# Optimization experiments

Hardware: AMD Instinct MI355X
Metric: run time of the kernel (lower is better)

## Reference

```python
import jax, jax.numpy as jnp
import numpy as np

N_NODES = 50000
N_EDGES = 800000
HID = 256
ATOM_F = 256
BOND_F = 128
BN_EPS = 1e-5


def setup_inputs() -> dict:
    key = jax.random.key(0)
    ks = jax.random.split(key, 8)
    x = jax.random.normal(ks[0], (N_NODES, ATOM_F), dtype=jnp.float32)
    w = jax.random.normal(ks[1], (N_EDGES, BOND_F), dtype=jnp.float32)
    dst = jax.random.randint(ks[2], (N_EDGES,), 0, N_NODES, dtype=jnp.int32)
    # Linear weights (PyTorch layout: [out, in]) scaled like kaiming-uniform-ish
    W_atom = jax.random.normal(ks[3], (HID, ATOM_F), dtype=jnp.float32) / np.sqrt(ATOM_F)
    b_atom = jax.random.normal(ks[4], (HID,), dtype=jnp.float32) * 0.01
    W_bond = jax.random.normal(ks[5], (HID, BOND_F), dtype=jnp.float32) / np.sqrt(BOND_F)
    b_bond = jax.random.normal(ks[6], (HID,), dtype=jnp.float32) * 0.01
    gamma = jnp.ones((HID,), dtype=jnp.float32)
    beta = jnp.zeros((HID,), dtype=jnp.float32)
    return {"x": x, "w": w, "dst": dst, "W_atom": W_atom, "b_atom": b_atom,
            "W_bond": W_bond, "b_bond": b_bond, "gamma": gamma, "beta": beta}


def reference(x, w, dst, W_atom, b_atom, W_bond, b_bond, gamma, beta):
    # Per-edge linear projection of bond features: [E, HID]
    h_edge = jnp.einsum('ef,hf->eh', w, W_bond) + b_bond
    # Scatter-sum messages into destination nodes: [N, HID]
    agg = jax.ops.segment_sum(h_edge, dst, num_segments=x.shape[0])
    # Node linear + add aggregated messages
    h = agg + jnp.einsum('nf,hf->nh', x, W_atom) + b_atom
    # ReLU then BatchNorm1d (training mode: biased batch stats, affine)
    h = jax.nn.relu(h)
    mean = jnp.mean(h, axis=0)
    var = jnp.mean(jnp.square(h - mean), axis=0)
    out = (h - mean) * jax.lax.rsqrt(var + BN_EPS) * gamma + beta
    return out
```

## Files before the change

### kernel.cpp

```cpp
#include <hip/hip_runtime.h>

#define NN 50000
#define NE 800000
#define HIDN 256
#define AF 256
#define BF 128
#define KT 384
#define NCHUNK 1563
#define GG 256
#define MAXDEG 128

typedef __attribute__((ext_vector_type(8))) short short8;
typedef __attribute__((ext_vector_type(4))) float f32x4;
typedef __attribute__((ext_vector_type(2))) float f32x2;

__device__ __forceinline__ unsigned short f2bf(float f) {
    union { float f; unsigned int u; } c; c.f = f;
    unsigned int u = c.u;
    return (unsigned short)((u + 0x7FFFu + ((u >> 16) & 1u)) >> 16);
}
__device__ __forceinline__ float bf2f(unsigned short u) {
    union { unsigned int u; float f; } c; c.u = (unsigned int)u << 16;
    return c.f;
}

__global__ __launch_bounds__(256) void k_sortW(const int4* __restrict__ dst4,
        int* __restrict__ cursor, int* __restrict__ sortedEdge,
        const float* __restrict__ Wa, const float* __restrict__ Wb,
        unsigned short* __restrict__ Wc) {
    const int i = blockIdx.x * 256 + threadIdx.x;
    if (i < NE / 4) {
        const int4 d = dst4[i];
        const int e = i * 4;
        int p;
        p = atomicAdd(cursor + d.x, 1); if (p < MAXDEG) sortedEdge[d.x * MAXDEG + p] = e;
        p = atomicAdd(cursor + d.y, 1); if (p < MAXDEG) sortedEdge[d.y * MAXDEG + p] = e + 1;
        p = atomicAdd(cursor + d.z, 1); if (p < MAXDEG) sortedEdge[d.z * MAXDEG + p] = e + 2;
        p = atomicAdd(cursor + d.w, 1); if (p < MAXDEG) sortedEdge[d.w * MAXDEG + p] = e + 3;
    }
    if (blockIdx.x < 48) {
        const int gid = blockIdx.x * 256 + threadIdx.x;
        const int j = gid / 48, cb = gid % 48;
        const float* src = (cb < 32) ? (Wa + j * AF + cb * 8) : (Wb + j * BF + (cb - 32) * 8);
        f32x4 a = reinterpret_cast<const f32x4*>(src)[0];
        f32x4 b = reinterpret_cast<const f32x4*>(src)[1];
        short8 s;
        s[0] = f2bf(a[0]); s[1] = f2bf(a[1]); s[2] = f2bf(a[2]); s[3] = f2bf(a[3]);
        s[4] = f2bf(b[0]); s[5] = f2bf(b[1]); s[6] = f2bf(b[2]); s[7] = f2bf(b[3]);
        *reinterpret_cast<short8*>(Wc + j * KT + cb * 8) = s;
    }
}

__global__ __launch_bounds__(256) void k_gather(const float* __restrict__ w,
        const int* __restrict__ sortedEdge, const int* __restrict__ cursor,
        unsigned short* __restrict__ agg) {
    const int node = blockIdx.x * 4 + (threadIdx.x >> 6);
    const int lane = threadIdx.x & 63;
    if (node >= NN) return;
    const int start = node * MAXDEG;
    const int degn = min(cursor[node], MAXDEG);
    const f32x2* __restrict__ w2 = reinterpret_cast<const f32x2*>(w);
    float ax = 0.f, ay = 0.f;
    for (int base = 0; base < degn; base += 64) {
        const int m = min(64, degn - base);
        int eid = 0;
        if (lane < m) eid = sortedEdge[start + base + lane];
        int i = 0;
        for (; i + 8 <= m; i += 8) {
            int e0 = __shfl(eid, i + 0), e1 = __shfl(eid, i + 1);
            int e2 = __shfl(eid, i + 2), e3 = __shfl(eid, i + 3);
            int e4 = __shfl(eid, i + 4), e5 = __shfl(eid, i + 5);
            int e6 = __shfl(eid, i + 6), e7 = __shfl(eid, i + 7);
            f32x2 v0 = __builtin_nontemporal_load(&w2[(size_t)e0 * 64 + lane]);
            f32x2 v1 = __builtin_nontemporal_load(&w2[(size_t)e1 * 64 + lane]);
            f32x2 v2 = __builtin_nontemporal_load(&w2[(size_t)e2 * 64 + lane]);
            f32x2 v3 = __builtin_nontemporal_load(&w2[(size_t)e3 * 64 + lane]);
            f32x2 v4 = __builtin_nontemporal_load(&w2[(size_t)e4 * 64 + lane]);
            f32x2 v5 = __builtin_nontemporal_load(&w2[(size_t)e5 * 64 + lane]);
            f32x2 v6 = __builtin_nontemporal_load(&w2[(size_t)e6 * 64 + lane]);
            f32x2 v7 = __builtin_nontemporal_load(&w2[(size_t)e7 * 64 + lane]);
            ax += ((v0.x + v1.x) + (v2.x + v3.x)) + ((v4.x + v5.x) + (v6.x + v7.x));
            ay += ((v0.y + v1.y) + (v2.y + v3.y)) + ((v4.y + v5.y) + (v6.y + v7.y));
        }
        for (; i < m; ++i) {
            int e = __shfl(eid, i);
            f32x2 v = __builtin_nontemporal_load(&w2[(size_t)e * 64 + lane]);
            ax += v.x;
            ay += v.y;
        }
    }
    unsigned int pack = (unsigned int)f2bf(ax) | ((unsigned int)f2bf(ay) << 16);
    *reinterpret_cast<unsigned int*>(agg + (size_t)node * BF + lane * 2) = pack;
}

#define LOADCHUNK(P, ch) do { \
    const int base_ = (ch) * 32; \
    const int g0_ = base_ + xr0, g1_ = g0_ + 16, g2_ = base_ + gr_; \
    if (g0_ < NN) { const f32x4* s_ = reinterpret_cast<const f32x4*>(x + (size_t)g0_ * AF + xkb * 8); \
        P##xa0 = __builtin_nontemporal_load(s_); P##xb0 = __builtin_nontemporal_load(s_ + 1); } \
    else { P##xa0 = f32x4{0.f,0.f,0.f,0.f}; P##xb0 = f32x4{0.f,0.f,0.f,0.f}; } \
    if (g1_ < NN) { const f32x4* s_ = reinterpret_cast<const f32x4*>(x + (size_t)g1_ * AF + xkb * 8); \
        P##xa1 = __builtin_nontemporal_load(s_); P##xb1 = __builtin_nontemporal_load(s_ + 1); } \
    else { P##xa1 = f32x4{0.f,0.f,0.f,0.f}; P##xb1 = f32x4{0.f,0.f,0.f,0.f}; } \
    if (g2_ < NN) { P##ga = *reinterpret_cast<const short8*>(agg + (size_t)g2_ * BF + gkb * 8); } \
    else { P##ga = short8{0,0,0,0,0,0,0,0}; } \
} while (0)

#define WRITECHUNK(P, BUF) do { \
    short8 s_; \
    s_[0]=f2bf(P##xa0[0]); s_[1]=f2bf(P##xa0[1]); s_[2]=f2bf(P##xa0[2]); s_[3]=f2bf(P##xa0[3]); \
    s_[4]=f2bf(P##xb0[0]); s_[5]=f2bf(P##xb0[1]); s_[6]=f2bf(P##xb0[2]); s_[7]=f2bf(P##xb0[3]); \
    *reinterpret_cast<short8*>((BUF) + xr0 * KT + ((xkb ^ (xr0 & 7)) << 3)) = s_; \
    s_[0]=f2bf(P##xa1[0]); s_[1]=f2bf(P##xa1[1]); s_[2]=f2bf(P##xa1[2]); s_[3]=f2bf(P##xa1[3]); \
    s_[4]=f2bf(P##xb1[0]); s_[5]=f2bf(P##xb1[1]); s_[6]=f2bf(P##xb1[2]); s_[7]=f2bf(P##xb1[3]); \
    *reinterpret_cast<short8*>((BUF) + (xr0 + 16) * KT + ((xkb ^ (xr0 & 7)) << 3)) = s_; \
    *reinterpret_cast<short8*>((BUF) + gr_ * KT + (((32 + gkb) ^ (gr_ & 7)) << 3)) = P##ga; \
} while (0)

__global__ __launch_bounds__(512, 1) void k_gemm(const float* __restrict__ x,
        const unsigned short* __restrict__ agg, const int* __restrict__ cnt,
        const unsigned short* __restrict__ Wc, const float* __restrict__ b_atom,
        const float* __restrict__ b_bond, unsigned short* __restrict__ hbf,
        float* __restrict__ colsum, float* __restrict__ colsumsq) {
    __shared__ unsigned short As0[32 * KT];
    __shared__ unsigned short As1[32 * KT];

    const int tid = threadIdx.x;
    const int wid = tid >> 6, lane = tid & 63;
    const int lrow = lane & 15, lk = lane >> 4;
    const int colb = wid * 32;

    short8 breg[2][12];
    #pragma unroll
    for (int t = 0; t < 2; ++t)
        #pragma unroll
        for (int kt = 0; kt < 12; ++kt)
            breg[t][kt] = *reinterpret_cast<const short8*>(
                Wc + (size_t)(colb + t * 16 + lrow) * KT + kt * 32 + lk * 8);

    const float ba0 = b_atom[colb + lrow],      bb0 = b_bond[colb + lrow];
    const float ba1 = b_atom[colb + 16 + lrow], bb1 = b_bond[colb + 16 + lrow];

    f32x4 Axa0, Axb0, Axa1, Axb1; short8 Aga;
    f32x4 Bxa0, Bxb0, Bxa1, Bxb1; short8 Bga;
    const int xr0 = tid >> 5, xkb = tid & 31;
    const int gr_ = tid >> 4, gkb = tid & 15;

    float st0 = 0.f, st20 = 0.f, st1 = 0.f, st21 = 0.f;

    auto compute = [&](int chunk, const unsigned short* A) {
        f32x4 a00{0.f,0.f,0.f,0.f}, a01{0.f,0.f,0.f,0.f};
        f32x4 a10{0.f,0.f,0.f,0.f}, a11{0.f,0.f,0.f,0.f};
        #pragma unroll
        for (int kt = 0; kt < 12; ++kt) {
            const int kb = kt * 4 + lk;
            short8 f0 = *reinterpret_cast<const short8*>(
                A + lrow * KT + ((kb ^ (lrow & 7)) << 3));
            short8 f1 = *reinterpret_cast<const short8*>(
                A + (16 + lrow) * KT + ((kb ^ (lrow & 7)) << 3));
            a00 = __builtin_amdgcn_mfma_f32_16x16x32_bf16(f0, breg[0][kt], a00, 0, 0, 0);
            a01 = __builtin_amdgcn_mfma_f32_16x16x32_bf16(f1, breg[0][kt], a01, 0, 0, 0);
            a10 = __builtin_amdgcn_mfma_f32_16x16x32_bf16(f0, breg[1][kt], a10, 0, 0, 0);
            a11 = __builtin_amdgcn_mfma_f32_16x16x32_bf16(f1, breg[1][kt], a11, 0, 0, 0);
        }
        #pragma unroll
        for (int rb = 0; rb < 2; ++rb) {
            const int row0 = chunk * 32 + rb * 16 + lk * 4;
            const f32x4 accA = rb ? a01 : a00;
            const f32x4 accB = rb ? a11 : a10;
            #pragma unroll
            for (int r2 = 0; r2 < 4; ++r2) {
                const int gr = row0 + r2;
                if (gr < NN) {
                    const float dg = (float)cnt[gr];
                    const float v0 = fmaxf(accA[r2] + ba0 + dg * bb0, 0.f);
                    const float v1 = fmaxf(accB[r2] + ba1 + dg * bb1, 0.f);
                    hbf[(size_t)gr * HIDN + colb + lrow]      = f2bf(v0);
                    hbf[(size_t)gr * HIDN + colb + 16 + lrow] = f2bf(v1);
                    st0 += v0; st20 += v0 * v0;
                    st1 += v1; st21 += v1 * v1;
                }
            }
        }
    };

    LOADCHUNK(A, blockIdx.x);
    WRITECHUNK(A, As0);
    LOADCHUNK(B, blockIdx.x + GG);
    asm volatile("s_waitcnt lgkmcnt(0)" ::: "memory");
    __builtin_amdgcn_s_barrier();

    int chunk = blockIdx.x;
    while (true) {
        WRITECHUNK(B, As1);
        LOADCHUNK(A, chunk + 2 * GG);
        compute(chunk, As0);
        asm volatile("s_waitcnt lgkmcnt(0)" ::: "memory");
        __builtin_amdgcn_s_barrier();
        chunk += GG;
        if (chunk >= NCHUNK) break;

        WRITECHUNK(A, As0);
        LOADCHUNK(B, chunk + 2 * GG);
        compute(chunk, As1);
        asm volatile("s_waitcnt lgkmcnt(0)" ::: "memory");
        __builtin_amdgcn_s_barrier();
        chunk += GG;
        if (chunk >= NCHUNK) break;
    }

    st0 += __shfl_xor(st0, 16); st0 += __shfl_xor(st0, 32);
    st20 += __shfl_xor(st20, 16); st20 += __shfl_xor(st20, 32);
    st1 += __shfl_xor(st1, 16); st1 += __shfl_xor(st1, 32);
    st21 += __shfl_xor(st21, 16); st21 += __shfl_xor(st21, 32);
    if (lane < 16) {
        atomicAdd(colsum + colb + lane, st0);
        atomicAdd(colsumsq + colb + lane, st20);
        atomicAdd(colsum + colb + 16 + lane, st1);
        atomicAdd(colsumsq + colb + 16 + lane, st21);
    }
}

__global__ __launch_bounds__(256) void k_bn(const unsigned short* __restrict__ hbf,
        const float* __restrict__ colsum, const float* __restrict__ colsumsq,
        const float* __restrict__ gamma, const float* __restrict__ beta,
        float* __restrict__ out) {
    __shared__ float scs[HIDN], shs[HIDN];
    const int t = threadIdx.x;
    {
        const float mean = colsum[t] * (1.f / NN);
        const float var = colsumsq[t] * (1.f / NN) - mean * mean;
        const float sc = gamma[t] * rsqrtf(var + 1e-5f);
        scs[t] = sc;
        shs[t] = beta[t] - mean * sc;
    }
    __syncthreads();
    const int total = NN * HIDN / 8;
    const short8* __restrict__ h8 = reinterpret_cast<const short8*>(hbf);
    f32x4* __restrict__ out4 = reinterpret_cast<f32x4*>(out);
    for (int gid = blockIdx.x * 256 + t; gid < total; gid += gridDim.x * 256) {
        const short8 v = __builtin_nontemporal_load(&h8[gid]);
        const int c = (gid & 31) * 8;
        f32x4 r0, r1;
        #pragma unroll
        for (int k = 0; k < 4; ++k)
            r0[k] = fmaf(bf2f((unsigned short)v[k]), scs[c + k], shs[c + k]);
        #pragma unroll
        for (int k = 0; k < 4; ++k)
            r1[k] = fmaf(bf2f((unsigned short)v[4 + k]), scs[c + 4 + k], shs[c + 4 + k]);
        __builtin_nontemporal_store(r0, &out4[gid * 2]);
        __builtin_nontemporal_store(r1, &out4[gid * 2 + 1]);
    }
}

extern "C" void kernel_launch(void* const* d_in, const int* in_sizes, int n_in,
                              void* d_out, int out_size, void* d_ws, size_t ws_size,
                              hipStream_t stream) {
    const float* x      = (const float*)d_in[0];
    const float* w      = (const float*)d_in[1];
    const int*   dst    = (const int*)d_in[2];
    const float* W_atom = (const float*)d_in[3];
    const float* b_atom = (const float*)d_in[4];
    const float* W_bond = (const float*)d_in[5];
    const float* b_bond = (const float*)d_in[6];
    const float* gamma  = (const float*)d_in[7];
    const float* beta   = (const float*)d_in[8];
    float* out = (float*)d_out;

    int*   cursor     = (int*)d_ws;
    float* colsum     = (float*)(cursor + NN);
    float* colsumsq   = colsum + HIDN;
    int*   sortedEdge = (int*)(colsumsq + HIDN);
    unsigned short* Wc  = (unsigned short*)(sortedEdge + (size_t)NN * MAXDEG);
    unsigned short* agg = Wc + (size_t)HIDN * KT;
    unsigned short* hbf = agg + (size_t)NN * BF;

    hipMemsetAsync(d_ws, 0, (size_t)(NN + 2 * HIDN) * 4, stream);

    k_sortW<<<(NE / 4 + 255) / 256, 256, 0, stream>>>((const int4*)dst, cursor,
                                                      sortedEdge, W_atom, W_bond, Wc);
    k_gather<<<(NN + 3) / 4, 256, 0, stream>>>(w, sortedEdge, cursor, agg);
    k_gemm<<<GG, 512, 0, stream>>>(x, agg, cursor, Wc, b_atom, b_bond,
                                   hbf, colsum, colsumsq);
    k_bn<<<2048, 256, 0, stream>>>(hbf, colsum, colsumsq, gamma, beta, out);
}
```

Baseline: 196.5 us.

## Fuse gather, GEMM and batchnorm into one persistent kernel with grid barriers

Replaces the separate gather, GEMM and BN kernels with a single persistent kernel of 256 blocks. Phases are separated by software grid barriers built on atomic counters. The aim is to remove two kernel launches and their tail idle gaps. In exchange, the gather phase runs with only 256 blocks of 8 waves at one block per CU, which may expose less memory-level parallelism than the original 12500-block launch. It also relies on every block being co-resident for the spin barrier.

```diff
diff --git a/kernel.cpp b/kernel.cpp
--- a/kernel.cpp
+++ b/kernel.cpp
@@ -7,7 +7,7 @@
 #define BF 128
 #define KT 384
 #define NCHUNK 1563
-#define GG 256
+#define NBLK 256
 #define MAXDEG 128
 
 typedef __attribute__((ext_vector_type(8))) short short8;
@@ -22,6 +22,18 @@
 __device__ __forceinline__ float bf2f(unsigned short u) {
     union { unsigned int u; float f; } c; c.u = (unsigned int)u << 16;
     return c.f;
+}
+
+__device__ __forceinline__ void grid_barrier(int* ctr) {
+    __syncthreads();
+    __threadfence();
+    if (threadIdx.x == 0) {
+        __hip_atomic_fetch_add(ctr, 1, __ATOMIC_ACQ_REL, __HIP_MEMORY_SCOPE_AGENT);
+        while (__hip_atomic_load(ctr, __ATOMIC_ACQUIRE, __HIP_MEMORY_SCOPE_AGENT) < NBLK) {
+            __builtin_amdgcn_s_sleep(2);
+        }
+    }
+    __syncthreads();
 }
 
 __global__ __launch_bounds__(256) void k_sortW(const int4* __restrict__ dst4,
@@ -51,48 +63,6 @@
     }
 }
 
-__global__ __launch_bounds__(256) void k_gather(const float* __restrict__ w,
-        const int* __restrict__ sortedEdge, const int* __restrict__ cursor,
-        unsigned short* __restrict__ agg) {
-    const int node = blockIdx.x * 4 + (threadIdx.x >> 6);
-    const int lane = threadIdx.x & 63;
-    if (node >= NN) return;
-    const int start = node * MAXDEG;
-    const int degn = min(cursor[node], MAXDEG);
-    const f32x2* __restrict__ w2 = reinterpret_cast<const f32x2*>(w);
-    float ax = 0.f, ay = 0.f;
-    for (int base = 0; base < degn; base += 64) {
-        const int m = min(64, degn - base);
-        int eid = 0;
-        if (lane < m) eid = sortedEdge[start + base + lane];
-        int i = 0;
-        for (; i + 8 <= m; i += 8) {
-            int e0 = __shfl(eid, i + 0), e1 = __shfl(eid, i + 1);
-            int e2 = __shfl(eid, i + 2), e3 = __shfl(eid, i + 3);
-            int e4 = __shfl(eid, i + 4), e5 = __shfl(eid, i + 5);
-            int e6 = __shfl(eid, i + 6), e7 = __shfl(eid, i + 7);
-            f32x2 v0 = __builtin_nontemporal_load(&w2[(size_t)e0 * 64 + lane]);
-            f32x2 v1 = __builtin_nontemporal_load(&w2[(size_t)e1 * 64 + lane]);
-            f32x2 v2 = __builtin_nontemporal_load(&w2[(size_t)e2 * 64 + lane]);
-            f32x2 v3 = __builtin_nontemporal_load(&w2[(size_t)e3 * 64 + lane]);
-            f32x2 v4 = __builtin_nontemporal_load(&w2[(size_t)e4 * 64 + lane]);
-            f32x2 v5 = __builtin_nontemporal_load(&w2[(size_t)e5 * 64 + lane]);
-            f32x2 v6 = __builtin_nontemporal_load(&w2[(size_t)e6 * 64 + lane]);
-            f32x2 v7 = __builtin_nontemporal_load(&w2[(size_t)e7 * 64 + lane]);
-            ax += ((v0.x + v1.x) + (v2.x + v3.x)) + ((v4.x + v5.x) + (v6.x + v7.x));
-            ay += ((v0.y + v1.y) + (v2.y + v3.y)) + ((v4.y + v5.y) + (v6.y + v7.y));
-        }
-        for (; i < m; ++i) {
-            int e = __shfl(eid, i);
-            f32x2 v = __builtin_nontemporal_load(&w2[(size_t)e * 64 + lane]);
-            ax += v.x;
-            ay += v.y;
-        }
-    }
-    unsigned int pack = (unsigned int)f2bf(ax) | ((unsigned int)f2bf(ay) << 16);
-    *reinterpret_cast<unsigned int*>(agg + (size_t)node * BF + lane * 2) = pack;
-}
-
 #define LOADCHUNK(P, ch) do { \
     const int base_ = (ch) * 32; \
     const int g0_ = base_ + xr0, g1_ = g0_ + 16, g2_ = base_ + gr_; \
@@ -117,139 +87,192 @@
     *reinterpret_cast<short8*>((BUF) + gr_ * KT + (((32 + gkb) ^ (gr_ & 7)) << 3)) = P##ga; \
 } while (0)
 
-__global__ __launch_bounds__(512, 1) void k_gemm(const float* __restrict__ x,
-        const unsigned short* __restrict__ agg, const int* __restrict__ cnt,
-        const unsigned short* __restrict__ Wc, const float* __restrict__ b_atom,
-        const float* __restrict__ b_bond, unsigned short* __restrict__ hbf,
-        float* __restrict__ colsum, float* __restrict__ colsumsq) {
+__global__ __launch_bounds__(512, 1) void k_mega(
+        const float* __restrict__ x, const float* __restrict__ w,
+        const int* __restrict__ sortedEdge, const int* __restrict__ cursor,
+        const unsigned short* __restrict__ Wc,
+        const float* __restrict__ b_atom, const float* __restrict__ b_bond,
+        const float* __restrict__ gamma, const float* __restrict__ beta,
+        unsigned short* __restrict__ agg, unsigned short* __restrict__ hbf,
+        float* __restrict__ colsum, float* __restrict__ colsumsq,
+        float* __restrict__ out, int* __restrict__ bar) {
     __shared__ unsigned short As0[32 * KT];
     __shared__ unsigned short As1[32 * KT];
-
-    const int tid = threadIdx.x;
+    __shared__ float scs[HIDN], shs[HIDN];
+
+    const int tid = threadIdx.x, bid = blockIdx.x;
     const int wid = tid >> 6, lane = tid & 63;
-    const int lrow = lane & 15, lk = lane >> 4;
-    const int colb = wid * 32;
-
-    short8 breg[2][12];
-    #pragma unroll
-    for (int t = 0; t < 2; ++t)
-        #pragma unroll
-        for (int kt = 0; kt < 12; ++kt)
-            breg[t][kt] = *reinterpret_cast<const short8*>(
-                Wc + (size_t)(colb + t * 16 + lrow) * KT + kt * 32 + lk * 8);
-
-    const float ba0 = b_atom[colb + lrow],      bb0 = b_bond[colb + lrow];
-    const float ba1 = b_atom[colb + 16 + lrow], bb1 = b_bond[colb + 16 + lrow];
-
-    f32x4 Axa0, Axb0, Axa1, Axb1; short8 Aga;
-    f32x4 Bxa0, Bxb0, Bxa1, Bxb1; short8 Bga;
-    const int xr0 = tid >> 5, xkb = tid & 31;
-    const int gr_ = tid >> 4, gkb = tid & 15;
-
-    float st0 = 0.f, st20 = 0.f, st1 = 0.f, st21 = 0.f;
-
-    auto compute = [&](int chunk, const unsigned short* A) {
-        f32x4 a00{0.f,0.f,0.f,0.f}, a01{0.f,0.f,0.f,0.f};
-        f32x4 a10{0.f,0.f,0.f,0.f}, a11{0.f,0.f,0.f,0.f};
-        #pragma unroll
-        for (int kt = 0; kt < 12; ++kt) {
-            const int kb = kt * 4 + lk;
-            short8 f0 = *reinterpret_cast<const short8*>(
-                A + lrow * KT + ((kb ^ (lrow & 7)) << 3));
-            short8 f1 = *reinterpret_cast<const short8*>(
-                A + (16 + lrow) * KT + ((kb ^ (lrow & 7)) << 3));
-            a00 = __builtin_amdgcn_mfma_f32_16x16x32_bf16(f0, breg[0][kt], a00, 0, 0, 0);
-            a01 = __builtin_amdgcn_mfma_f32_16x16x32_bf16(f1, breg[0][kt], a01, 0, 0, 0);
-            a10 = __builtin_amdgcn_mfma_f32_16x16x32_bf16(f0, breg[1][kt], a10, 0, 0, 0);
-            a11 = __builtin_amdgcn_mfma_f32_16x16x32_bf16(f1, breg[1][kt], a11, 0, 0, 0);
-        }
-        #pragma unroll
-        for (int rb = 0; rb < 2; ++rb) {
-            const int row0 = chunk * 32 + rb * 16 + lk * 4;
-            const f32x4 accA = rb ? a01 : a00;
-            const f32x4 accB = rb ? a11 : a10;
-            #pragma unroll
-            for (int r2 = 0; r2 < 4; ++r2) {
-                const int gr = row0 + r2;
-                if (gr < NN) {
-                    const float dg = (float)cnt[gr];
-                    const float v0 = fmaxf(accA[r2] + ba0 + dg * bb0, 0.f);
-                    const float v1 = fmaxf(accB[r2] + ba1 + dg * bb1, 0.f);
-                    hbf[(size_t)gr * HIDN + colb + lrow]      = f2bf(v0);
-                    hbf[(size_t)gr * HIDN + colb + 16 + lrow] = f2bf(v1);
-                    st0 += v0; st20 += v0 * v0;
-                    st1 += v1; st21 += v1 * v1;
+
+    {
+        const f32x2* __restrict__ w2 = reinterpret_cast<const f32x2*>(w);
+        for (int node = bid * 8 + wid; node < NN; node += NBLK * 8) {
+            const int start = node * MAXDEG;
+            const int degn = min(cursor[node], MAXDEG);
+            float ax = 0.f, ay = 0.f;
+            for (int base = 0; base < degn; base += 64) {
+                const int m = min(64, degn - base);
+                int eid = 0;
+                if (lane < m) eid = sortedEdge[start + base + lane];
+                int i = 0;
+                for (; i + 8 <= m; i += 8) {
+                    int e0 = __shfl(eid, i + 0), e1 = __shfl(eid, i + 1);
+                    int e2 = __shfl(eid, i + 2), e3 = __shfl(eid, i + 3);
+                    int e4 = __shfl(eid, i + 4), e5 = __shfl(eid, i + 5);
+                    int e6 = __shfl(eid, i + 6), e7 = __shfl(eid, i + 7);
+                    f32x2 v0 = __builtin_nontemporal_load(&w2[(size_t)e0 * 64 + lane]);
+                    f32x2 v1 = __builtin_nontemporal_load(&w2[(size_t)e1 * 64 + lane]);
+                    f32x2 v2 = __builtin_nontemporal_load(&w2[(size_t)e2 * 64 + lane]);
+                    f32x2 v3 = __builtin_nontemporal_load(&w2[(size_t)e3 * 64 + lane]);
+                    f32x2 v4 = __builtin_nontemporal_load(&w2[(size_t)e4 * 64 + lane]);
+                    f32x2 v5 = __builtin_nontemporal_load(&w2[(size_t)e5 * 64 + lane]);
+                    f32x2 v6 = __builtin_nontemporal_load(&w2[(size_t)e6 * 64 + lane]);
+                    f32x2 v7 = __builtin_nontemporal_load(&w2[(size_t)e7 * 64 + lane]);
+                    ax += ((v0.x + v1.x) + (v2.x + v3.x)) + ((v4.x + v5.x) + (v6.x + v7.x));
+                    ay += ((v0.y + v1.y) + (v2.y + v3.y)) + ((v4.y + v5.y) + (v6.y + v7.y));
+                }
+                for (; i < m; ++i) {
+                    int e = __shfl(eid, i);
+                    f32x2 v = __builtin_nontemporal_load(&w2[(size_t)e * 64 + lane]);
+                    ax += v.x;
+                    ay += v.y;
                 }
             }
-        }
-    };
-
-    LOADCHUNK(A, blockIdx.x);
-    WRITECHUNK(A, As0);
-    LOADCHUNK(B, blockIdx.x + GG);
-    asm volatile("s_waitcnt lgkmcnt(0)" ::: "memory");
-    __builtin_amdgcn_s_barrier();
-
-    int chunk = blockIdx.x;
-    while (true) {
-        WRITECHUNK(B, As1);
-        LOADCHUNK(A, chunk + 2 * GG);
-        compute(chunk, As0);
+            unsigned int pack = (unsigned int)f2bf(ax) | ((unsigned int)f2bf(ay) << 16);
+            *reinterpret_cast<unsigned int*>(agg + (size_t)node * BF + lane * 2) = pack;
+        }
+    }
+    grid_barrier(bar + 0);
+
+    {
+        const int* __restrict__ cnt = cursor;
+        const int lrow = lane & 15, lk = lane >> 4;
+        const int colb = wid * 32;
+
+        short8 breg[2][12];
+        #pragma unroll
+        for (int t = 0; t < 2; ++t)
+            #pragma unroll
+            for (int kt = 0; kt < 12; ++kt)
+                breg[t][kt] = *reinterpret_cast<const short8*>(
+                    Wc + (size_t)(colb + t * 16 + lrow) * KT + kt * 32 + lk * 8);
+
+        const float ba0 = b_atom[colb + lrow],      bb0 = b_bond[colb + lrow];
+        const float ba1 = b_atom[colb + 16 + lrow], bb1 = b_bond[colb + 16 + lrow];
+
+        f32x4 Axa0, Axb0, Axa1, Axb1; short8 Aga;
+        f32x4 Bxa0, Bxb0, Bxa1, Bxb1; short8 Bga;
+        const int xr0 = tid >> 5, xkb = tid & 31;
+        const int gr_ = tid >> 4, gkb = tid & 15;
+
+        float st0 = 0.f, st20 = 0.f, st1 = 0.f, st21 = 0.f;
+
+        auto compute = [&](int chunk, const unsigned short* A) {
+            f32x4 a00{0.f,0.f,0.f,0.f}, a01{0.f,0.f,0.f,0.f};
+            f32x4 a10{0.f,0.f,0.f,0.f}, a11{0.f,0.f,0.f,0.f};
+            #pragma unroll
+            for (int kt = 0; kt < 12; ++kt) {
+                const int kb = kt * 4 + lk;
+                short8 f0 = *reinterpret_cast<const short8*>(
+                    A + lrow * KT + ((kb ^ (lrow & 7)) << 3));
+                short8 f1 = *reinterpret_cast<const short8*>(
+                    A + (16 + lrow) * KT + ((kb ^ (lrow & 7)) << 3));
+                a00 = __builtin_amdgcn_mfma_f32_16x16x32_bf16(f0, breg[0][kt], a00, 0, 0, 0);
+                a01 = __builtin_amdgcn_mfma_f32_16x16x32_bf16(f1, breg[0][kt], a01, 0, 0, 0);
+                a10 = __builtin_amdgcn_mfma_f32_16x16x32_bf16(f0, breg[1][kt], a10, 0, 0, 0);
+                a11 = __builtin_amdgcn_mfma_f32_16x16x32_bf16(f1, breg[1][kt], a11, 0, 0, 0);
+            }
+            #pragma unroll
+            for (int rb = 0; rb < 2; ++rb) {
+                const int row0 = chunk * 32 + rb * 16 + lk * 4;
+                const f32x4 accA = rb ? a01 : a00;
+                const f32x4 accB = rb ? a11 : a10;
+                #pragma unroll
+                for (int r2 = 0; r2 < 4; ++r2) {
+                    const int gr = row0 + r2;
+                    if (gr < NN) {
+                        const float dg = (float)cnt[gr];
+                        const float v0 = fmaxf(accA[r2] + ba0 + dg * bb0, 0.f);
+                        const float v1 = fmaxf(accB[r2] + ba1 + dg * bb1, 0.f);
+                        hbf[(size_t)gr * HIDN + colb + lrow]      = f2bf(v0);
+                        hbf[(size_t)gr * HIDN + colb + 16 + lrow] = f2bf(v1);
+                        st0 += v0; st20 += v0 * v0;
+                        st1 += v1; st21 += v1 * v1;
+                    }
+                }
+            }
+        };
+
+        LOADCHUNK(A, bid);
+        WRITECHUNK(A, As0);
+        LOADCHUNK(B, bid + NBLK);
         asm volatile("s_waitcnt lgkmcnt(0)" ::: "memory");
         __builtin_amdgcn_s_barrier();
-        chunk += GG;
-        if (chunk >= NCHUNK) break;
-
-        WRITECHUNK(A, As0);
-        LOADCHUNK(B, chunk + 2 * GG);
-        compute(chunk, As1);
-        asm volatile("s_waitcnt lgkmcnt(0)" ::: "memory");
-        __builtin_amdgcn_s_barrier();
-        chunk += GG;
-        if (chunk >= NCHUNK) break;
-    }
-
-    st0 += __shfl_xor(st0, 16); st0 += __shfl_xor(st0, 32);
-    st20 += __shfl_xor(st20, 16); st20 += __shfl_xor(st20, 32);
-    st1 += __shfl_xor(st1, 16); st1 += __shfl_xor(st1, 32);
-    st21 += __shfl_xor(st21, 16); st21 += __shfl_xor(st21, 32);
-    if (lane < 16) {
-        atomicAdd(colsum + colb + lane, st0);
-        atomicAdd(colsumsq + colb + lane, st20);
-        atomicAdd(colsum + colb + 16 + lane, st1);
-        atomicAdd(colsumsq + colb + 16 + lane, st21);
-    }
-}
-
-__global__ __launch_bounds__(256) void k_bn(const unsigned short* __restrict__ hbf,
-        const float* __restrict__ colsum, const float* __restrict__ colsumsq,
-        const float* __restrict__ gamma, const float* __restrict__ beta,
-        float* __restrict__ out) {
-    __shared__ float scs[HIDN], shs[HIDN];
-    const int t = threadIdx.x;
+
+        int chunk = bid;
+        while (true) {
+            WRITECHUNK(B, As1);
+            LOADCHUNK(A, chunk + 2 * NBLK);
+            compute(chunk, As0);
+            asm volatile("s_waitcnt lgkmcnt(0)" ::: "memory");
+            __builtin_amdgcn_s_barrier();
+            chunk += NBLK;
+            if (chunk >= NCHUNK) break;
+
+            WRITECHUNK(A, As0);
+            LOADCHUNK(B, chunk + 2 * NBLK);
+            compute(chunk, As1);
+            asm volatile("s_waitcnt lgkmcnt(0)" ::: "memory");
+            __builtin_amdgcn_s_barrier();
+            chunk += NBLK;
+            if (chunk >= NCHUNK) break;
+        }
+
+        st0 += __shfl_xor(st0, 16); st0 += __shfl_xor(st0, 32);
+        st20 += __shfl_xor(st20, 16); st20 += __shfl_xor(st20, 32);
+        st1 += __shfl_xor(st1, 16); st1 += __shfl_xor(st1, 32);
+        st21 += __shfl_xor(st21, 16); st21 += __shfl_xor(st21, 32);
+        if (lane < 16) {
+            atomicAdd(colsum + colb + lane, st0);
+            atomicAdd(colsumsq + colb + lane, st20);
+            atomicAdd(colsum + colb + 16 + lane, st1);
+            atomicAdd(colsumsq + colb + 16 + lane, st21);
+        }
+    }
+    grid_barrier(bar + 1);
+
+    if (tid < HIDN) {
+        const float cs = __hip_atomic_load(&colsum[tid], __ATOMIC_RELAXED, __HIP_MEMORY_SCOPE_AGENT);
+        const float cq = __hip_atomic_load(&colsumsq[tid], __ATOMIC_RELAXED, __HIP_MEMORY_SCOPE_AGENT);
+        const float mean = cs * (1.f / NN);
+        const float var = cq * (1.f / NN) - mean * mean;
+        const float sc = gamma[tid] * rsqrtf(var + 1e-5f);
+        scs[tid] = sc;
+        shs[tid] = beta[tid] - mean * sc;
+    }
+    __syncthreads();
     {
-        const float mean = colsum[t] * (1.f / NN);
-        const float var = colsumsq[t] * (1.f / NN) - mean * mean;
-        const float sc = gamma[t] * rsqrtf(var + 1e-5f);
-        scs[t] = sc;
-        shs[t] = beta[t] - mean * sc;
-    }
-    __syncthreads();
-    const int total = NN * HIDN / 8;
-    const short8* __restrict__ h8 = reinterpret_cast<const short8*>(hbf);
-    f32x4* __restrict__ out4 = reinterpret_cast<f32x4*>(out);
-    for (int gid = blockIdx.x * 256 + t; gid < total; gid += gridDim.x * 256) {
-        const short8 v = __builtin_nontemporal_load(&h8[gid]);
-        const int c = (gid & 31) * 8;
-        f32x4 r0, r1;
-        #pragma unroll
-        for (int k = 0; k < 4; ++k)
-            r0[k] = fmaf(bf2f((unsigned short)v[k]), scs[c + k], shs[c + k]);
-        #pragma unroll
-        for (int k = 0; k < 4; ++k)
-            r1[k] = fmaf(bf2f((unsigned short)v[4 + k]), scs[c + 4 + k], shs[c + 4 + k]);
-        __builtin_nontemporal_store(r0, &out4[gid * 2]);
-        __builtin_nontemporal_store(r1, &out4[gid * 2 + 1]);
+        const short8* __restrict__ h8 = reinterpret_cast<const short8*>(hbf);
+        f32x4* __restrict__ out4 = reinterpret_cast<f32x4*>(out);
+        for (int c = bid; c < NCHUNK; c += NBLK) {
+            const int base8 = c * 1024;
+            #pragma unroll
+            for (int k = 0; k < 2; ++k) {
+                const int g = base8 + k * 512 + tid;
+                if (g < NN * 32) {
+                    const short8 v = __builtin_nontemporal_load(&h8[g]);
+                    const int cc = (g & 31) * 8;
+                    f32x4 r0, r1;
+                    #pragma unroll
+                    for (int q = 0; q < 4; ++q)
+                        r0[q] = fmaf(bf2f((unsigned short)v[q]), scs[cc + q], shs[cc + q]);
+                    #pragma unroll
+                    for (int q = 0; q < 4; ++q)
+                        r1[q] = fmaf(bf2f((unsigned short)v[4 + q]), scs[cc + 4 + q], shs[cc + 4 + q]);
+                    __builtin_nontemporal_store(r0, &out4[(size_t)g * 2]);
+                    __builtin_nontemporal_store(r1, &out4[(size_t)g * 2 + 1]);
+                }
+            }
+        }
     }
 }
 
@@ -270,17 +293,17 @@
     int*   cursor     = (int*)d_ws;
     float* colsum     = (float*)(cursor + NN);
     float* colsumsq   = colsum + HIDN;
-    int*   sortedEdge = (int*)(colsumsq + HIDN);
+    int*   bar        = (int*)(colsumsq + HIDN);
+    int*   sortedEdge = bar + 8;
     unsigned short* Wc  = (unsigned short*)(sortedEdge + (size_t)NN * MAXDEG);
     unsigned short* agg = Wc + (size_t)HIDN * KT;
     unsigned short* hbf = agg + (size_t)NN * BF;
 
-    hipMemsetAsync(d_ws, 0, (size_t)(NN + 2 * HIDN) * 4, stream);
+    hipMemsetAsync(d_ws, 0, (size_t)(NN + 2 * HIDN + 8) * 4, stream);
 
     k_sortW<<<(NE / 4 + 255) / 256, 256, 0, stream>>>((const int4*)dst, cursor,
                                                       sortedEdge, W_atom, W_bond, Wc);
-    k_gather<<<(NN + 3) / 4, 256, 0, stream>>>(w, sortedEdge, cursor, agg);
-    k_gemm<<<GG, 512, 0, stream>>>(x, agg, cursor, Wc, b_atom, b_bond,
-                                   hbf, colsum, colsumsq);
-    k_bn<<<2048, 256, 0, stream>>>(hbf, colsum, colsumsq, gamma, beta, out);
-}
+    k_mega<<<NBLK, 512, 0, stream>>>(x, w, sortedEdge, cursor, Wc,
+                                     b_atom, b_bond, gamma, beta,
+                                     agg, hbf, colsum, colsumsq, out, bar);
+}
```

New measurement: 360.5 us. +83.4%, slower.

## Double GEMM row tile to 64 rows and simplify prefetch pipeline to one-ahead

Applied to the files above, without the earlier changes.

The fused node GEMM now processes 64-row chunks instead of 32. Each wave reuses its register-resident weight fragments across four row tiles, giving more MFMA work per LDS A-fragment load and per barrier. The two-deep register prefetch (A/B sets) is replaced by a single set loaded one chunk ahead, with LDS double buffering kept. This doubles LDS use and accumulator registers, and leaves fewer chunks (782) spread over 256 blocks, which worsens the tail imbalance.

```diff
diff --git a/kernel.cpp b/kernel.cpp
--- a/kernel.cpp
+++ b/kernel.cpp
@@ -6,7 +6,7 @@
 #define AF 256
 #define BF 128
 #define KT 384
-#define NCHUNK 1563
+#define NCH64 782
 #define GG 256
 #define MAXDEG 128
 
@@ -93,28 +93,43 @@
     *reinterpret_cast<unsigned int*>(agg + (size_t)node * BF + lane * 2) = pack;
 }
 
-#define LOADCHUNK(P, ch) do { \
-    const int base_ = (ch) * 32; \
-    const int g0_ = base_ + xr0, g1_ = g0_ + 16, g2_ = base_ + gr_; \
+#define LOADCH(ch) do { \
+    const int base_ = (ch) * 64; \
+    const int g0_ = base_ + xr0; \
     if (g0_ < NN) { const f32x4* s_ = reinterpret_cast<const f32x4*>(x + (size_t)g0_ * AF + xkb * 8); \
-        P##xa0 = __builtin_nontemporal_load(s_); P##xb0 = __builtin_nontemporal_load(s_ + 1); } \
-    else { P##xa0 = f32x4{0.f,0.f,0.f,0.f}; P##xb0 = f32x4{0.f,0.f,0.f,0.f}; } \
-    if (g1_ < NN) { const f32x4* s_ = reinterpret_cast<const f32x4*>(x + (size_t)g1_ * AF + xkb * 8); \
-        P##xa1 = __builtin_nontemporal_load(s_); P##xb1 = __builtin_nontemporal_load(s_ + 1); } \
-    else { P##xa1 = f32x4{0.f,0.f,0.f,0.f}; P##xb1 = f32x4{0.f,0.f,0.f,0.f}; } \
-    if (g2_ < NN) { P##ga = *reinterpret_cast<const short8*>(agg + (size_t)g2_ * BF + gkb * 8); } \
-    else { P##ga = short8{0,0,0,0,0,0,0,0}; } \
+        xa0 = __builtin_nontemporal_load(s_); xb0 = __builtin_nontemporal_load(s_ + 1); } \
+    else { xa0 = f32x4{0.f,0.f,0.f,0.f}; xb0 = f32x4{0.f,0.f,0.f,0.f}; } \
+    if (g0_ + 16 < NN) { const f32x4* s_ = reinterpret_cast<const f32x4*>(x + (size_t)(g0_ + 16) * AF + xkb * 8); \
+        xa1 = __builtin_nontemporal_load(s_); xb1 = __builtin_nontemporal_load(s_ + 1); } \
+    else { xa1 = f32x4{0.f,0.f,0.f,0.f}; xb1 = f32x4{0.f,0.f,0.f,0.f}; } \
+    if (g0_ + 32 < NN) { const f32x4* s_ = reinterpret_cast<const f32x4*>(x + (size_t)(g0_ + 32) * AF + xkb * 8); \
+        xa2 = __builtin_nontemporal_load(s_); xb2 = __builtin_nontemporal_load(s_ + 1); } \
+    else { xa2 = f32x4{0.f,0.f,0.f,0.f}; xb2 = f32x4{0.f,0.f,0.f,0.f}; } \
+    if (g0_ + 48 < NN) { const f32x4* s_ = reinterpret_cast<const f32x4*>(x + (size_t)(g0_ + 48) * AF + xkb * 8); \
+        xa3 = __builtin_nontemporal_load(s_); xb3 = __builtin_nontemporal_load(s_ + 1); } \
+    else { xa3 = f32x4{0.f,0.f,0.f,0.f}; xb3 = f32x4{0.f,0.f,0.f,0.f}; } \
+    const int g2_ = base_ + gr_; \
+    if (g2_ < NN) { ga0 = *reinterpret_cast<const short8*>(agg + (size_t)g2_ * BF + gkb * 8); } \
+    else { ga0 = short8{0,0,0,0,0,0,0,0}; } \
+    if (g2_ + 32 < NN) { ga1 = *reinterpret_cast<const short8*>(agg + (size_t)(g2_ + 32) * BF + gkb * 8); } \
+    else { ga1 = short8{0,0,0,0,0,0,0,0}; } \
 } while (0)
 
-#define WRITECHUNK(P, BUF) do { \
+#define WRROW(XA, XB, ROW) do { \
     short8 s_; \
-    s_[0]=f2bf(P##xa0[0]); s_[1]=f2bf(P##xa0[1]); s_[2]=f2bf(P##xa0[2]); s_[3]=f2bf(P##xa0[3]); \
-    s_[4]=f2bf(P##xb0[0]); s_[5]=f2bf(P##xb0[1]); s_[6]=f2bf(P##xb0[2]); s_[7]=f2bf(P##xb0[3]); \
-    *reinterpret_cast<short8*>((BUF) + xr0 * KT + ((xkb ^ (xr0 & 7)) << 3)) = s_; \
-    s_[0]=f2bf(P##xa1[0]); s_[1]=f2bf(P##xa1[1]); s_[2]=f2bf(P##xa1[2]); s_[3]=f2bf(P##xa1[3]); \
-    s_[4]=f2bf(P##xb1[0]); s_[5]=f2bf(P##xb1[1]); s_[6]=f2bf(P##xb1[2]); s_[7]=f2bf(P##xb1[3]); \
-    *reinterpret_cast<short8*>((BUF) + (xr0 + 16) * KT + ((xkb ^ (xr0 & 7)) << 3)) = s_; \
-    *reinterpret_cast<short8*>((BUF) + gr_ * KT + (((32 + gkb) ^ (gr_ & 7)) << 3)) = P##ga; \
+    s_[0]=f2bf(XA[0]); s_[1]=f2bf(XA[1]); s_[2]=f2bf(XA[2]); s_[3]=f2bf(XA[3]); \
+    s_[4]=f2bf(XB[0]); s_[5]=f2bf(XB[1]); s_[6]=f2bf(XB[2]); s_[7]=f2bf(XB[3]); \
+    *reinterpret_cast<short8*>(BUF + (ROW) * KT + ((xkb ^ ((ROW) & 7)) << 3)) = s_; \
+} while (0)
+
+#define WRITECH(B_) do { \
+    unsigned short* BUF = (B_); \
+    WRROW(xa0, xb0, xr0); \
+    WRROW(xa1, xb1, xr0 + 16); \
+    WRROW(xa2, xb2, xr0 + 32); \
+    WRROW(xa3, xb3, xr0 + 48); \
+    *reinterpret_cast<short8*>(BUF + gr_ * KT + (((32 + gkb) ^ (gr_ & 7)) << 3)) = ga0; \
+    *reinterpret_cast<short8*>(BUF + (gr_ + 32) * KT + (((32 + gkb) ^ ((gr_ + 32) & 7)) << 3)) = ga1; \
 } while (0)
 
 __global__ __launch_bounds__(512, 1) void k_gemm(const float* __restrict__ x,
@@ -122,8 +137,8 @@
         const unsigned short* __restrict__ Wc, const float* __restrict__ b_atom,
         const float* __restrict__ b_bond, unsigned short* __restrict__ hbf,
         float* __restrict__ colsum, float* __restrict__ colsumsq) {
-    __shared__ unsigned short As0[32 * KT];
-    __shared__ unsigned short As1[32 * KT];
+    __shared__ unsigned short As0[64 * KT];
+    __shared__ unsigned short As1[64 * KT];
 
     const int tid = threadIdx.x;
     const int wid = tid >> 6, lane = tid & 63;
@@ -141,40 +156,42 @@
     const float ba0 = b_atom[colb + lrow],      bb0 = b_bond[colb + lrow];
     const float ba1 = b_atom[colb + 16 + lrow], bb1 = b_bond[colb + 16 + lrow];
 
-    f32x4 Axa0, Axb0, Axa1, Axb1; short8 Aga;
-    f32x4 Bxa0, Bxb0, Bxa1, Bxb1; short8 Bga;
+    f32x4 xa0, xb0, xa1, xb1, xa2, xb2, xa3, xb3;
+    short8 ga0, ga1;
     const int xr0 = tid >> 5, xkb = tid & 31;
     const int gr_ = tid >> 4, gkb = tid & 15;
 
     float st0 = 0.f, st20 = 0.f, st1 = 0.f, st21 = 0.f;
 
     auto compute = [&](int chunk, const unsigned short* A) {
-        f32x4 a00{0.f,0.f,0.f,0.f}, a01{0.f,0.f,0.f,0.f};
-        f32x4 a10{0.f,0.f,0.f,0.f}, a11{0.f,0.f,0.f,0.f};
+        f32x4 acc[4][2];
+        #pragma unroll
+        for (int rt = 0; rt < 4; ++rt) {
+            acc[rt][0] = f32x4{0.f,0.f,0.f,0.f};
+            acc[rt][1] = f32x4{0.f,0.f,0.f,0.f};
+        }
         #pragma unroll
         for (int kt = 0; kt < 12; ++kt) {
             const int kb = kt * 4 + lk;
-            short8 f0 = *reinterpret_cast<const short8*>(
-                A + lrow * KT + ((kb ^ (lrow & 7)) << 3));
-            short8 f1 = *reinterpret_cast<const short8*>(
-                A + (16 + lrow) * KT + ((kb ^ (lrow & 7)) << 3));
-            a00 = __builtin_amdgcn_mfma_f32_16x16x32_bf16(f0, breg[0][kt], a00, 0, 0, 0);
-            a01 = __builtin_amdgcn_mfma_f32_16x16x32_bf16(f1, breg[0][kt], a01, 0, 0, 0);
-            a10 = __builtin_amdgcn_mfma_f32_16x16x32_bf16(f0, breg[1][kt], a10, 0, 0, 0);
-            a11 = __builtin_amdgcn_mfma_f32_16x16x32_bf16(f1, breg[1][kt], a11, 0, 0, 0);
-        }
-        #pragma unroll
-        for (int rb = 0; rb < 2; ++rb) {
-            const int row0 = chunk * 32 + rb * 16 + lk * 4;
-            const f32x4 accA = rb ? a01 : a00;
-            const f32x4 accB = rb ? a11 : a10;
+            const int so = (kb ^ (lrow & 7)) << 3;
+            #pragma unroll
+            for (int rt = 0; rt < 4; ++rt) {
+                short8 f = *reinterpret_cast<const short8*>(
+                    A + (rt * 16 + lrow) * KT + so);
+                acc[rt][0] = __builtin_amdgcn_mfma_f32_16x16x32_bf16(f, breg[0][kt], acc[rt][0], 0, 0, 0);
+                acc[rt][1] = __builtin_amdgcn_mfma_f32_16x16x32_bf16(f, breg[1][kt], acc[rt][1], 0, 0, 0);
+            }
+        }
+        #pragma unroll
+        for (int rt = 0; rt < 4; ++rt) {
+            const int row0 = chunk * 64 + rt * 16 + lk * 4;
             #pragma unroll
             for (int r2 = 0; r2 < 4; ++r2) {
                 const int gr = row0 + r2;
                 if (gr < NN) {
                     const float dg = (float)cnt[gr];
-                    const float v0 = fmaxf(accA[r2] + ba0 + dg * bb0, 0.f);
-                    const float v1 = fmaxf(accB[r2] + ba1 + dg * bb1, 0.f);
+                    const float v0 = fmaxf(acc[rt][0][r2] + ba0 + dg * bb0, 0.f);
+                    const float v1 = fmaxf(acc[rt][1][r2] + ba1 + dg * bb1, 0.f);
                     hbf[(size_t)gr * HIDN + colb + lrow]      = f2bf(v0);
                     hbf[(size_t)gr * HIDN + colb + 16 + lrow] = f2bf(v1);
                     st0 += v0; st20 += v0 * v0;
@@ -184,29 +201,23 @@
         }
     };
 
-    LOADCHUNK(A, blockIdx.x);
-    WRITECHUNK(A, As0);
-    LOADCHUNK(B, blockIdx.x + GG);
+    LOADCH(blockIdx.x);
+    WRITECH(As0);
     asm volatile("s_waitcnt lgkmcnt(0)" ::: "memory");
     __builtin_amdgcn_s_barrier();
 
     int chunk = blockIdx.x;
+    int buf = 0;
     while (true) {
-        WRITECHUNK(B, As1);
-        LOADCHUNK(A, chunk + 2 * GG);
-        compute(chunk, As0);
+        const bool more = (chunk + GG < NCH64);
+        if (more) LOADCH(chunk + GG);
+        compute(chunk, buf ? As1 : As0);
+        if (!more) break;
+        WRITECH(buf ? As0 : As1);
         asm volatile("s_waitcnt lgkmcnt(0)" ::: "memory");
         __builtin_amdgcn_s_barrier();
         chunk += GG;
-        if (chunk >= NCHUNK) break;
-
-        WRITECHUNK(A, As0);
-        LOADCHUNK(B, chunk + 2 * GG);
-        compute(chunk, As1);
-        asm volatile("s_waitcnt lgkmcnt(0)" ::: "memory");
-        __builtin_amdgcn_s_barrier();
-        chunk += GG;
-        if (chunk >= NCHUNK) break;
+        buf ^= 1;
     }
 
     st0 += __shfl_xor(st0, 16); st0 += __shfl_xor(st0, 32);
```

After: 194.8 us. About the same (-0.8%).
